# Performance work log

Measured on AMD Instinct MI355X. Metric: run time of the kernel, lower is better.

Reference implementation:

```python
import jax, jax.numpy as jnp
import numpy as np

N, E, L = 20000, 640000, 2
D_IN, D_H, D_FF = 1546, 128, 512  # in_channels, heads*out_channels, ff_dim
EPS = 1e-5
SLOPE = 0.01  # LeakyReLU default negative slope


def layer_norm(x, g, b):
    m = x.mean(-1, keepdims=True)
    v = ((x - m) ** 2).mean(-1, keepdims=True)
    return (x - m) / jnp.sqrt(v + EPS) * g + b


def setup_inputs() -> dict:
    key = jax.random.key(0)
    ks = iter(jax.random.split(key, 40))
    f32 = jnp.float32
    def w(shape, scale=0.05):
        return jax.random.normal(next(ks), shape, dtype=f32) * scale
    inp = {
        "x": jax.random.normal(next(ks), (N, D_IN), dtype=f32),
        "edge_index": jax.random.randint(next(ks), (2, E), 0, N, dtype=jnp.int64),
        "edge_attr": jax.random.normal(next(ks), (E, D_H), dtype=f32),
        # per-layer TransformerConv params, stacked over L layers
        "Wq": w((L, D_IN, D_H)), "bq": jnp.zeros((L, D_H), f32),
        "Wk": w((L, D_IN, D_H)), "bk": jnp.zeros((L, D_H), f32),
        "Wv": w((L, D_IN, D_H)), "bv": jnp.zeros((L, D_H), f32),
        "Wr": w((L, D_IN, D_H)), "br": jnp.zeros((L, D_H), f32),
        "Whi": w((L, D_IN, D_H)), "Whj": w((L, D_IN, D_H)),
        # per-layer FFMLP params
        "W1": w((L, D_H, D_FF)), "b1": jnp.zeros((L, D_FF), f32),
        "W2": w((L, D_FF, D_H)), "b2": jnp.zeros((L, D_H), f32),
        "g1": jnp.ones((L, D_H), f32), "be1": jnp.zeros((L, D_H), f32),
        "g2": jnp.ones((L, D_H), f32), "be2": jnp.zeros((L, D_H), f32),
        # shared linear 128->1546 and final linear2 1546->128
        "linW": w((D_H, D_IN)), "linb": jnp.zeros((D_IN,), f32),
        "lin2W": w((D_IN, D_H)), "lin2b": jnp.zeros((D_H,), f32),
    }
    return inp


def reference(x, edge_index, edge_attr, Wq, bq, Wk, bk, Wv, bv, Wr, br,
              Whi, Whj, W1, b1, W2, b2, g1, be1, g2, be2,
              linW, linb, lin2W, lin2b):
    src = edge_index[0]  # j (source)
    dst = edge_index[1]  # i (target)
    for l in range(L):
        q = x @ Wq[l] + bq[l]          # [N, D_H]
        k = x @ Wk[l] + bk[l]
        v = x @ Wv[l] + bv[l]
        hi = x @ Whi[l]
        hj = x @ Whj[l]
        # edge gate (uses raw edge_attr, matching original forward)
        gate = jax.nn.sigmoid(edge_attr + hi[src] + hj[dst])      # [E, D_H]
        # per-edge scalar attention, softmax over ALL edges (dim=0, as in source)
        attn = jnp.sum(q[dst] * k[src], axis=-1, keepdims=True)   # [E, 1]
        attn = jax.nn.softmax(attn, axis=0)
        msg = attn * v[src] * gate                                 # [E, D_H]
        aggr = jax.ops.segment_sum(msg, dst, num_segments=N)       # [N, D_H]
        h = aggr + x @ Wr[l] + br[l]   # root weight, concat=False -> no out_proj
        # FFMLP (pre-norm residual on normalized input)
        ss = layer_norm(h, g1[l], be1[l])
        ss2 = jax.nn.relu(ss @ W1[l] + b1[l]) @ W2[l] + b2[l]
        h = layer_norm(ss + ss2, g2[l], be2[l])
        x = h @ linW + linb            # shared 128 -> 1546
    x = jax.nn.leaky_relu(x @ lin2W + lin2b, SLOPE)
    return x
```

## Files before the change

kernel.cpp:

```cpp
#include <hip/hip_runtime.h>
#include <cfloat>
#include <cmath>

#define NN 20000
#define EE 640000
#define DIN 1546
#define KIN 1568
#define DH 128
#define DFF 512
#define NL 2
#define NPROJ 768
#define LINNP 1664
#define LINNS 1568
#define ALB 2048

typedef unsigned short ushort_t;
typedef __attribute__((ext_vector_type(8))) short short8;
typedef __attribute__((ext_vector_type(8))) unsigned short ushort8;
typedef __attribute__((ext_vector_type(4))) float floatx4;

__device__ inline ushort_t f2bf(float f) {
  unsigned u = __float_as_uint(f);
  unsigned r = (u + 0x7FFF + ((u >> 16) & 1)) >> 16;
  return (ushort_t)r;
}
__device__ inline float bflo(unsigned u) { return __uint_as_float(u << 16); }
__device__ inline float bfhi(unsigned u) { return __uint_as_float(u & 0xFFFF0000u); }

__global__ __launch_bounds__(256) void gemm_bf16(
    const ushort_t* __restrict__ A, int lda,
    const ushort_t* __restrict__ Bt, int ldb,
    const float* __restrict__ bias, void* __restrict__ Cv, int ldc,
    int M, int Nstore, int K, int act, int out_bf16)
{
  __shared__ ushort_t As[4 * 1032];
  __shared__ ushort_t Bs[4 * 1032];
  const int tid = threadIdx.x;
  const int wave = tid >> 6, lane = tid & 63;
  const int bm = blockIdx.x * 128, bn = blockIdx.y * 128;
  const int wm = (wave >> 1) * 64, wn = (wave & 1) * 64;
  const int frow = lane & 15, kq = lane >> 4;

  floatx4 acc[4][4];
  #pragma unroll
  for (int i = 0; i < 4; ++i)
    #pragma unroll
    for (int j = 0; j < 4; ++j) acc[i][j] = (floatx4){0.f, 0.f, 0.f, 0.f};

  const int srow = tid >> 2, skc = tid & 3;
  const int ar0 = min(bm + srow, M - 1);
  const int ar1 = min(bm + srow + 64, M - 1);
  const ushort_t* Ap0 = A + (size_t)ar0 * lda + skc * 8;
  const ushort_t* Ap1 = A + (size_t)ar1 * lda + skc * 8;
  const ushort_t* Bp0 = Bt + (size_t)(bn + srow) * ldb + skc * 8;
  const ushort_t* Bp1 = Bt + (size_t)(bn + srow + 64) * ldb + skc * 8;
  ushort_t* Aw0 = As + skc * 1032 + srow * 8;
  ushort_t* Aw1 = As + skc * 1032 + (srow + 64) * 8;
  ushort_t* Bw0 = Bs + skc * 1032 + srow * 8;
  ushort_t* Bw1 = Bs + skc * 1032 + (srow + 64) * 8;

  for (int k0 = 0; k0 < K; k0 += 32) {
    ushort8 a0 = *(const ushort8*)Ap0; Ap0 += 32;
    ushort8 a1 = *(const ushort8*)Ap1; Ap1 += 32;
    ushort8 b0 = *(const ushort8*)Bp0; Bp0 += 32;
    ushort8 b1 = *(const ushort8*)Bp1; Bp1 += 32;
    __syncthreads();
    *(ushort8*)Aw0 = a0; *(ushort8*)Aw1 = a1;
    *(ushort8*)Bw0 = b0; *(ushort8*)Bw1 = b1;
    __syncthreads();
    short8 af[4], bf[4];
    #pragma unroll
    for (int i = 0; i < 4; ++i)
      af[i] = *(const short8*)(As + kq * 1032 + (wm + i * 16 + frow) * 8);
    #pragma unroll
    for (int j = 0; j < 4; ++j)
      bf[j] = *(const short8*)(Bs + kq * 1032 + (wn + j * 16 + frow) * 8);
    #pragma unroll
    for (int i = 0; i < 4; ++i)
      #pragma unroll
      for (int j = 0; j < 4; ++j)
        acc[i][j] = __builtin_amdgcn_mfma_f32_16x16x32_bf16(af[i], bf[j], acc[i][j], 0, 0, 0);
  }

  const int rq = (lane >> 4) * 4;
  #pragma unroll
  for (int j = 0; j < 4; ++j) {
    int col = bn + wn + j * 16 + frow;
    if (col >= Nstore) continue;
    float bb = bias ? bias[col] : 0.f;
    #pragma unroll
    for (int i = 0; i < 4; ++i) {
      #pragma unroll
      for (int r = 0; r < 4; ++r) {
        int row = bm + wm + i * 16 + rq + r;
        if (row >= M) continue;
        float v = acc[i][j][r] + bb;
        if (act == 1) v = fmaxf(v, 0.f);
        else if (act == 2) v = v > 0.f ? v : 0.01f * v;
        if (out_bf16) ((ushort_t*)Cv)[(size_t)row * ldc + col] = f2bf(v);
        else          ((float*)Cv)[(size_t)row * ldc + col] = v;
      }
    }
  }
}

__global__ void convert_x_kernel(const float* __restrict__ x, ushort_t* __restrict__ xb) {
  int c = blockIdx.x * 256 + threadIdx.x;
  int row = blockIdx.y;
  if (c >= KIN) return;
  xb[(size_t)row * KIN + c] = (c < DIN) ? f2bf(x[(size_t)row * DIN + c]) : (ushort_t)0;
}

__global__ void pack6_kernel(const float* __restrict__ Wq, const float* __restrict__ Wk,
                             const float* __restrict__ Wv, const float* __restrict__ Wr,
                             const float* __restrict__ Whi, const float* __restrict__ Whj,
                             ushort_t* __restrict__ Wt6) {
  int k = blockIdx.x * 256 + threadIdx.x;
  int n = blockIdx.y;
  if (k >= KIN) return;
  const float* W[6] = {Wq, Wk, Wv, Wr, Whi, Whj};
  int which = n >> 7, col = n & 127;
  float v = (k < DIN) ? W[which][(size_t)k * DH + col] : 0.f;
  Wt6[(size_t)n * KIN + k] = f2bf(v);
}

__global__ void pack_bt_kernel(const float* __restrict__ src, ushort_t* __restrict__ dst,
                               int Nsrc, int Ksrc, int Kp) {
  int k = blockIdx.x * 256 + threadIdx.x;
  int n = blockIdx.y;
  if (k >= Kp) return;
  float v = (n < Nsrc && k < Ksrc) ? src[(size_t)k * Nsrc + n] : 0.f;
  dst[(size_t)n * Kp + k] = f2bf(v);
}

__global__ void pack_bias_kernel(const float* __restrict__ bq, const float* __restrict__ bk,
                                 const float* __restrict__ bv, const float* __restrict__ br,
                                 float* __restrict__ out) {
  int n = blockIdx.x * 256 + threadIdx.x;
  if (n >= NPROJ) return;
  int which = n >> 7, c = n & 127;
  float v = 0.f;
  if (which == 0) v = bq[c]; else if (which == 1) v = bk[c];
  else if (which == 2) v = bv[c]; else if (which == 3) v = br[c];
  out[n] = v;
}

__global__ void pad_linb_kernel(const float* __restrict__ linb, float* __restrict__ out) {
  int n = blockIdx.x * 256 + threadIdx.x;
  if (n >= LINNS) return;
  out[n] = (n < DIN) ? linb[n] : 0.f;
}

__global__ void hist_kernel(const int* __restrict__ ei, int* __restrict__ counts) {
  int e = blockIdx.x * 256 + threadIdx.x;
  if (e < EE) atomicAdd(&counts[ei[EE + e]], 1);
}

__global__ __launch_bounds__(1024) void scan_kernel(const int* __restrict__ counts,
                                                    int* __restrict__ offsets,
                                                    int* __restrict__ cursor) {
  __shared__ int sums[1024];
  const int t = threadIdx.x;
  const int PER = 20;
  int base = t * PER;
  int loc[PER]; int s = 0;
  #pragma unroll
  for (int i = 0; i < PER; ++i) {
    int idx = base + i;
    int c = (idx < NN) ? counts[idx] : 0;
    loc[i] = s; s += c;
  }
  sums[t] = s;
  __syncthreads();
  for (int d = 1; d < 1024; d <<= 1) {
    int v = (t >= d) ? sums[t - d] : 0;
    __syncthreads();
    sums[t] += v;
    __syncthreads();
  }
  int pre = (t > 0) ? sums[t - 1] : 0;
  #pragma unroll
  for (int i = 0; i < PER; ++i) {
    int idx = base + i;
    if (idx < NN) { offsets[idx] = pre + loc[i]; cursor[idx] = pre + loc[i]; }
  }
  if (t == 0) offsets[NN] = sums[1023];
}

__global__ void scatter_kernel(const int* __restrict__ ei, int* __restrict__ cursor,
                               int* __restrict__ csr) {
  int e = blockIdx.x * 256 + threadIdx.x;
  if (e < EE) {
    int p = atomicAdd(&cursor[ei[EE + e]], 1);
    csr[p] = e;
  }
}

__device__ inline void atomicMaxF(float* addr, float val) {
  if (val >= 0.f) atomicMax((int*)addr, __float_as_int(val));
  else            atomicMin((unsigned int*)addr, __float_as_uint(val));
}

__global__ void init_scalars(float* scal) {
  if (threadIdx.x == 0) { scal[0] = -INFINITY; scal[1] = 0.f; }
}

__global__ __launch_bounds__(256) void attn_logits(
    const int* __restrict__ ei, const ushort_t* __restrict__ qkv,
    float* __restrict__ s_e, float* __restrict__ scal)
{
  const int tid = threadIdx.x;
  const int l = tid & 31;
  const int ngroups = ALB * 8;
  const int g = blockIdx.x * 8 + (tid >> 5);
  float mx = -FLT_MAX;
  for (int e = g; e < EE; e += 2 * ngroups) {
    const int e2 = e + ngroups;
    const bool has2 = (e2 < EE);
    int src1 = ei[e], dst1 = ei[EE + e];
    int src2 = has2 ? ei[e2] : src1;
    int dst2 = has2 ? ei[EE + e2] : dst1;
    uint2 qu1 = *(const uint2*)(qkv + (size_t)dst1 * NPROJ + l * 4);
    uint2 ku1 = *(const uint2*)(qkv + (size_t)src1 * NPROJ + DH + l * 4);
    uint2 qu2 = *(const uint2*)(qkv + (size_t)dst2 * NPROJ + l * 4);
    uint2 ku2 = *(const uint2*)(qkv + (size_t)src2 * NPROJ + DH + l * 4);
    float d1 = bflo(qu1.x) * bflo(ku1.x) + bfhi(qu1.x) * bfhi(ku1.x)
             + bflo(qu1.y) * bflo(ku1.y) + bfhi(qu1.y) * bfhi(ku1.y);
    float d2 = bflo(qu2.x) * bflo(ku2.x) + bfhi(qu2.x) * bfhi(ku2.x)
             + bflo(qu2.y) * bflo(ku2.y) + bfhi(qu2.y) * bfhi(ku2.y);
    #pragma unroll
    for (int m = 16; m >= 1; m >>= 1) {
      d1 += __shfl_xor(d1, m);
      d2 += __shfl_xor(d2, m);
    }
    if (l == 0) {
      s_e[e] = d1;
      if (has2) s_e[e2] = d2;
    }
    mx = fmaxf(mx, has2 ? fmaxf(d1, d2) : d1);
  }
  mx = fmaxf(mx, __shfl_xor(mx, 32));
  __shared__ float red[4];
  if ((tid & 63) == 0) red[tid >> 6] = mx;
  __syncthreads();
  if (tid == 0)
    atomicMaxF(scal, fmaxf(fmaxf(red[0], red[1]), fmaxf(red[2], red[3])));
}

__global__ __launch_bounds__(256) void exp_sum(
    float* __restrict__ s_e, const float* __restrict__ scal, float* __restrict__ Z)
{
  const int e = blockIdx.x * 256 + threadIdx.x;
  const float mx = scal[0];
  float v = __expf(s_e[e] - mx);
  s_e[e] = v;
  float t = v;
  #pragma unroll
  for (int m = 32; m >= 1; m >>= 1) t += __shfl_xor(t, m);
  __shared__ float red[4];
  if ((threadIdx.x & 63) == 0) red[threadIdx.x >> 6] = t;
  __syncthreads();
  if (threadIdx.x == 0) atomicAdd(Z, red[0] + red[1] + red[2] + red[3]);
}

__global__ __launch_bounds__(256) void aggregate_kernel(
    const int* __restrict__ ei, const int* __restrict__ offsets,
    const int* __restrict__ csr, const float* __restrict__ s_e,
    const float* __restrict__ scal, const ushort_t* __restrict__ qkv,
    const float* __restrict__ ea, float* __restrict__ h)
{
  const int node = blockIdx.x * 4 + (threadIdx.x >> 6);
  const int lane = threadIdx.x & 63;
  if (node >= NN) return;
  const int off = offsets[node];
  const int deg = offsets[node + 1] - off;
  const float invZ = 1.f / scal[1];
  const ushort_t* bd = qkv + (size_t)node * NPROJ;
  unsigned hjp = *(const unsigned*)(bd + 640 + lane * 2);
  unsigned rp  = *(const unsigned*)(bd + 384 + lane * 2);
  const float hj0 = bflo(hjp), hj1 = bfhi(hjp);
  float a0 = bflo(rp), a1 = bfhi(rp);
  for (int b0 = 0; b0 < deg; b0 += 64) {
    int t = b0 + lane;
    int eL = (t < deg) ? csr[off + t] : 0;
    int sL = (t < deg) ? ei[eL] : 0;
    float pL = (t < deg) ? s_e[eL] * invZ : 0.f;
    int cnt = min(64, deg - b0);
    for (int u = 0; u < cnt; ++u) {
      int e = __shfl(eL, u);
      int src = __shfl(sL, u);
      float p = __shfl(pL, u);
      const ushort_t* bs = qkv + (size_t)src * NPROJ;
      unsigned vv = *(const unsigned*)(bs + 256 + lane * 2);
      unsigned hv = *(const unsigned*)(bs + 512 + lane * 2);
      float2 eav = *(const float2*)(ea + (size_t)e * DH + lane * 2);
      float g0 = 1.f / (1.f + __expf(-(eav.x + bflo(hv) + hj0)));
      float g1 = 1.f / (1.f + __expf(-(eav.y + bfhi(hv) + hj1)));
      a0 = fmaf(p * bflo(vv), g0, a0);
      a1 = fmaf(p * bfhi(vv), g1, a1);
    }
  }
  *(float2*)(h + (size_t)node * DH + lane * 2) = make_float2(a0, a1);
}

__global__ __launch_bounds__(256) void ln_kernel(
    const float* __restrict__ X, const float* __restrict__ X2,
    const float* __restrict__ g, const float* __restrict__ b,
    float* __restrict__ Yf, ushort_t* __restrict__ Yb)
{
  int row = blockIdx.x * 4 + (threadIdx.x >> 6);
  int lane = threadIdx.x & 63;
  if (row >= NN) return;
  float2 x = *(const float2*)(X + (size_t)row * DH + lane * 2);
  if (X2) {
    float2 y = *(const float2*)(X2 + (size_t)row * DH + lane * 2);
    x.x += y.x; x.y += y.y;
  }
  float s = x.x + x.y;
  #pragma unroll
  for (int m = 32; m >= 1; m >>= 1) s += __shfl_xor(s, m);
  float mean = s * (1.f / 128.f);
  float dx = x.x - mean, dy = x.y - mean;
  float v = dx * dx + dy * dy;
  #pragma unroll
  for (int m = 32; m >= 1; m >>= 1) v += __shfl_xor(v, m);
  float rstd = rsqrtf(v * (1.f / 128.f) + 1e-5f);
  float2 gg = *(const float2*)(g + lane * 2);
  float2 bb = *(const float2*)(b + lane * 2);
  float o0 = dx * rstd * gg.x + bb.x;
  float o1 = dy * rstd * gg.y + bb.y;
  if (Yf) *(float2*)(Yf + (size_t)row * DH + lane * 2) = make_float2(o0, o1);
  if (Yb) {
    ushort_t* p = Yb + (size_t)row * DH + lane * 2;
    p[0] = f2bf(o0); p[1] = f2bf(o1);
  }
}

extern "C" void kernel_launch(void* const* d_in, const int* in_sizes, int n_in,
                              void* d_out, int out_size, void* d_ws, size_t ws_size,
                              hipStream_t stream)
{
  const float* x_in  = (const float*)d_in[0];
  const int*   ei    = (const int*)d_in[1];
  const float* ea    = (const float*)d_in[2];
  const float* Wq    = (const float*)d_in[3];
  const float* bq    = (const float*)d_in[4];
  const float* Wk    = (const float*)d_in[5];
  const float* bk    = (const float*)d_in[6];
  const float* Wv    = (const float*)d_in[7];
  const float* bv    = (const float*)d_in[8];
  const float* Wr    = (const float*)d_in[9];
  const float* br    = (const float*)d_in[10];
  const float* Whi   = (const float*)d_in[11];
  const float* Whj   = (const float*)d_in[12];
  const float* W1    = (const float*)d_in[13];
  const float* b1    = (const float*)d_in[14];
  const float* W2    = (const float*)d_in[15];
  const float* b2    = (const float*)d_in[16];
  const float* g1    = (const float*)d_in[17];
  const float* be1   = (const float*)d_in[18];
  const float* g2    = (const float*)d_in[19];
  const float* be2   = (const float*)d_in[20];
  const float* linW  = (const float*)d_in[21];
  const float* linb  = (const float*)d_in[22];
  const float* lin2W = (const float*)d_in[23];
  const float* lin2b = (const float*)d_in[24];
  float* out = (float*)d_out;

  char* p = (char*)d_ws;
  auto alloc = [&](size_t bytes) -> void* {
    void* r = (void*)p; p += (bytes + 63) & ~((size_t)63); return r;
  };
  ushort_t* x_bf   = (ushort_t*)alloc((size_t)NN * KIN * 2);
  ushort_t* qkvp   = (ushort_t*)alloc((size_t)NN * NPROJ * 2);
  ushort_t* Wt6    = (ushort_t*)alloc((size_t)NPROJ * KIN * 2);
  ushort_t* W1t    = (ushort_t*)alloc((size_t)DFF * DH * 2);
  ushort_t* W2t    = (ushort_t*)alloc((size_t)DH * DFF * 2);
  ushort_t* lint   = (ushort_t*)alloc((size_t)LINNP * DH * 2);
  ushort_t* lin2t  = (ushort_t*)alloc((size_t)DH * KIN * 2);
  float*    bias768= (float*)alloc(NPROJ * 4);
  float*    linbp  = (float*)alloc(LINNS * 4);
  float*    s_e    = (float*)alloc((size_t)EE * 4);
  float*    scal   = (float*)alloc(64);
  int*      counts = (int*)alloc((size_t)NN * 4);
  int*      offsets= (int*)alloc((size_t)(NN + 1) * 4);
  int*      cursor = (int*)alloc((size_t)NN * 4);
  int*      csr    = (int*)alloc((size_t)EE * 4);
  float*    h      = (float*)alloc((size_t)NN * DH * 4);
  float*    ss     = (float*)alloc((size_t)NN * DH * 4);
  ushort_t* ssbf   = (ushort_t*)alloc((size_t)NN * DH * 2);
  ushort_t* ff1bf  = (ushort_t*)alloc((size_t)NN * DFF * 2);
  float*    ss2    = (float*)alloc((size_t)NN * DH * 4);
  ushort_t* h2bf   = (ushort_t*)alloc((size_t)NN * DH * 2);

  const dim3 blk(256);
  const int MB = (NN + 127) / 128;

  convert_x_kernel<<<dim3(7, NN), blk, 0, stream>>>(x_in, x_bf);
  pack_bt_kernel<<<dim3(1, LINNP), blk, 0, stream>>>(linW, lint, DIN, DH, DH);
  pack_bt_kernel<<<dim3(7, DH), blk, 0, stream>>>(lin2W, lin2t, DH, DIN, KIN);
  pad_linb_kernel<<<dim3(7), blk, 0, stream>>>(linb, linbp);
  hipMemsetAsync(counts, 0, (size_t)NN * 4, stream);
  hist_kernel<<<dim3(EE / 256), blk, 0, stream>>>(ei, counts);
  scan_kernel<<<dim3(1), dim3(1024), 0, stream>>>(counts, offsets, cursor);
  scatter_kernel<<<dim3(EE / 256), blk, 0, stream>>>(ei, cursor, csr);

  for (int l = 0; l < NL; ++l) {
    const size_t wo = (size_t)l * DIN * DH;
    pack6_kernel<<<dim3(7, NPROJ), blk, 0, stream>>>(
        Wq + wo, Wk + wo, Wv + wo, Wr + wo, Whi + wo, Whj + wo, Wt6);
    pack_bias_kernel<<<dim3(3), blk, 0, stream>>>(
        bq + (size_t)l * DH, bk + (size_t)l * DH, bv + (size_t)l * DH, br + (size_t)l * DH, bias768);
    pack_bt_kernel<<<dim3(1, DFF), blk, 0, stream>>>(W1 + (size_t)l * DH * DFF, W1t, DFF, DH, DH);
    pack_bt_kernel<<<dim3(2, DH), blk, 0, stream>>>(W2 + (size_t)l * DFF * DH, W2t, DH, DFF, DFF);

    gemm_bf16<<<dim3(MB, 6), blk, 0, stream>>>(
        x_bf, KIN, Wt6, KIN, bias768, qkvp, NPROJ, NN, NPROJ, KIN, 0, 1);

    init_scalars<<<1, 64, 0, stream>>>(scal);
    attn_logits<<<dim3(ALB), blk, 0, stream>>>(ei, qkvp, s_e, scal);
    exp_sum<<<dim3(EE / 256), blk, 0, stream>>>(s_e, scal, scal + 1);
    aggregate_kernel<<<dim3(NN / 4), blk, 0, stream>>>(
        ei, offsets, csr, s_e, scal, qkvp, ea, h);

    ln_kernel<<<dim3(NN / 4), blk, 0, stream>>>(h, nullptr, g1 + (size_t)l * DH, be1 + (size_t)l * DH, ss, ssbf);
    gemm_bf16<<<dim3(MB, 4), blk, 0, stream>>>(
        ssbf, DH, W1t, DH, b1 + (size_t)l * DFF, ff1bf, DFF, NN, DFF, DH, 1, 1);
    gemm_bf16<<<dim3(MB, 1), blk, 0, stream>>>(
        ff1bf, DFF, W2t, DFF, b2 + (size_t)l * DH, ss2, DH, NN, DH, DFF, 0, 0);
    ln_kernel<<<dim3(NN / 4), blk, 0, stream>>>(ss, ss2, g2 + (size_t)l * DH, be2 + (size_t)l * DH, nullptr, h2bf);

    gemm_bf16<<<dim3(MB, 13), blk, 0, stream>>>(
        h2bf, DH, lint, DH, linbp, x_bf, KIN, NN, LINNS, DH, 0, 1);
  }

  gemm_bf16<<<dim3(MB, 1), blk, 0, stream>>>(
      x_bf, KIN, lin2t, KIN, lin2b, out, DH, NN, DH, KIN, 2, 0);
}
```

Baseline: 1.610 ms.

## Fold shared 128->1546 linear into following projection weights

Precomputes combined weights linW·W for the layer-1 projections and linW·lin2W for the final linear, including combined biases. The wide 1546-column intermediate x is no longer materialised after each layer. The layer-2 projection GEMM and the final GEMM then run with K=128 instead of K=1568. This removes two large GEMMs and their traffic, at the cost of small weight-combination kernels and different bf16 rounding of the folded weights.

Result: no change. 1.585 ms (-1.5%).

```diff
diff --git a/kernel.cpp b/kernel.cpp
--- a/kernel.cpp
+++ b/kernel.cpp
@@ -10,8 +10,6 @@
 #define DFF 512
 #define NL 2
 #define NPROJ 768
-#define LINNP 1664
-#define LINNS 1568
 #define ALB 2048
 
 typedef unsigned short ushort_t;
@@ -145,10 +143,78 @@
   out[n] = v;
 }
 
-__global__ void pad_linb_kernel(const float* __restrict__ linb, float* __restrict__ out) {
-  int n = blockIdx.x * 256 + threadIdx.x;
-  if (n >= LINNS) return;
-  out[n] = (n < DIN) ? linb[n] : 0.f;
+__global__ __launch_bounds__(256) void combine6_kernel(
+    const float* __restrict__ Wq, const float* __restrict__ Wk,
+    const float* __restrict__ Wv, const float* __restrict__ Wr,
+    const float* __restrict__ Whi, const float* __restrict__ Whj,
+    const float* __restrict__ bq, const float* __restrict__ bk,
+    const float* __restrict__ bv, const float* __restrict__ br,
+    const float* __restrict__ linW, const float* __restrict__ linb,
+    ushort_t* __restrict__ Pc, float* __restrict__ bc)
+{
+  const int j = threadIdx.x >> 7;
+  const int k = threadIdx.x & 127;
+  const int n = blockIdx.x * 2 + j;
+  const int which = n >> 7, col = n & 127;
+  const float* Ws[6] = {Wq, Wk, Wv, Wr, Whi, Whj};
+  const float* W = Ws[which];
+  __shared__ float wcol[2][DIN];
+  for (int d = k; d < DIN; d += 128)
+    wcol[j][d] = W[(size_t)d * DH + col];
+  __syncthreads();
+  const float* lr = linW + (size_t)k * DIN;
+  float acc = 0.f;
+  #pragma unroll 4
+  for (int d = 0; d < DIN; d += 2) {
+    float2 lv = *(const float2*)(lr + d);
+    acc = fmaf(wcol[j][d], lv.x, acc);
+    acc = fmaf(wcol[j][d + 1], lv.y, acc);
+  }
+  Pc[(size_t)n * DH + k] = f2bf(acc);
+  float bs = 0.f;
+  for (int d = k; d < DIN; d += 128) bs += linb[d] * wcol[j][d];
+  #pragma unroll
+  for (int m = 32; m >= 1; m >>= 1) bs += __shfl_xor(bs, m);
+  __shared__ float red[4];
+  if ((threadIdx.x & 63) == 0) red[threadIdx.x >> 6] = bs;
+  __syncthreads();
+  if (k == 0) {
+    float b0 = 0.f;
+    if (which == 0) b0 = bq[col]; else if (which == 1) b0 = bk[col];
+    else if (which == 2) b0 = bv[col]; else if (which == 3) b0 = br[col];
+    bc[n] = b0 + red[j * 2] + red[j * 2 + 1];
+  }
+}
+
+__global__ __launch_bounds__(256) void combine_fin_kernel(
+    const float* __restrict__ lin2W, const float* __restrict__ lin2b,
+    const float* __restrict__ linW, const float* __restrict__ linb,
+    ushort_t* __restrict__ Pf, float* __restrict__ bf_out)
+{
+  const int j = threadIdx.x >> 7;
+  const int k = threadIdx.x & 127;
+  const int c = blockIdx.x * 2 + j;
+  __shared__ float wcol[2][DIN];
+  for (int d = k; d < DIN; d += 128)
+    wcol[j][d] = lin2W[(size_t)d * DH + c];
+  __syncthreads();
+  const float* lr = linW + (size_t)k * DIN;
+  float acc = 0.f;
+  #pragma unroll 4
+  for (int d = 0; d < DIN; d += 2) {
+    float2 lv = *(const float2*)(lr + d);
+    acc = fmaf(wcol[j][d], lv.x, acc);
+    acc = fmaf(wcol[j][d + 1], lv.y, acc);
+  }
+  Pf[(size_t)c * DH + k] = f2bf(acc);
+  float bs = 0.f;
+  for (int d = k; d < DIN; d += 128) bs += linb[d] * wcol[j][d];
+  #pragma unroll
+  for (int m = 32; m >= 1; m >>= 1) bs += __shfl_xor(bs, m);
+  __shared__ float red[4];
+  if ((threadIdx.x & 63) == 0) red[threadIdx.x >> 6] = bs;
+  __syncthreads();
+  if (k == 0) bf_out[c] = lin2b[c] + red[j * 2] + red[j * 2 + 1];
 }
 
 __global__ void hist_kernel(const int* __restrict__ ei, int* __restrict__ counts) {
@@ -376,10 +442,11 @@
   ushort_t* Wt6    = (ushort_t*)alloc((size_t)NPROJ * KIN * 2);
   ushort_t* W1t    = (ushort_t*)alloc((size_t)DFF * DH * 2);
   ushort_t* W2t    = (ushort_t*)alloc((size_t)DH * DFF * 2);
-  ushort_t* lint   = (ushort_t*)alloc((size_t)LINNP * DH * 2);
-  ushort_t* lin2t  = (ushort_t*)alloc((size_t)DH * KIN * 2);
+  ushort_t* Wc6    = (ushort_t*)alloc((size_t)NPROJ * DH * 2);
+  ushort_t* Wcf    = (ushort_t*)alloc((size_t)DH * DH * 2);
   float*    bias768= (float*)alloc(NPROJ * 4);
-  float*    linbp  = (float*)alloc(LINNS * 4);
+  float*    bc768  = (float*)alloc(NPROJ * 4);
+  float*    bcf    = (float*)alloc(DH * 4);
   float*    s_e    = (float*)alloc((size_t)EE * 4);
   float*    scal   = (float*)alloc(64);
   int*      counts = (int*)alloc((size_t)NN * 4);
@@ -397,25 +464,32 @@
   const int MB = (NN + 127) / 128;
 
   convert_x_kernel<<<dim3(7, NN), blk, 0, stream>>>(x_in, x_bf);
-  pack_bt_kernel<<<dim3(1, LINNP), blk, 0, stream>>>(linW, lint, DIN, DH, DH);
-  pack_bt_kernel<<<dim3(7, DH), blk, 0, stream>>>(lin2W, lin2t, DH, DIN, KIN);
-  pad_linb_kernel<<<dim3(7), blk, 0, stream>>>(linb, linbp);
   hipMemsetAsync(counts, 0, (size_t)NN * 4, stream);
   hist_kernel<<<dim3(EE / 256), blk, 0, stream>>>(ei, counts);
   scan_kernel<<<dim3(1), dim3(1024), 0, stream>>>(counts, offsets, cursor);
   scatter_kernel<<<dim3(EE / 256), blk, 0, stream>>>(ei, cursor, csr);
 
+  const size_t wo1 = (size_t)DIN * DH;
+  combine6_kernel<<<dim3(NPROJ / 2), blk, 0, stream>>>(
+      Wq + wo1, Wk + wo1, Wv + wo1, Wr + wo1, Whi + wo1, Whj + wo1,
+      bq + DH, bk + DH, bv + DH, br + DH, linW, linb, Wc6, bc768);
+  combine_fin_kernel<<<dim3(DH / 2), blk, 0, stream>>>(
+      lin2W, lin2b, linW, linb, Wcf, bcf);
+
   for (int l = 0; l < NL; ++l) {
-    const size_t wo = (size_t)l * DIN * DH;
-    pack6_kernel<<<dim3(7, NPROJ), blk, 0, stream>>>(
-        Wq + wo, Wk + wo, Wv + wo, Wr + wo, Whi + wo, Whj + wo, Wt6);
-    pack_bias_kernel<<<dim3(3), blk, 0, stream>>>(
-        bq + (size_t)l * DH, bk + (size_t)l * DH, bv + (size_t)l * DH, br + (size_t)l * DH, bias768);
     pack_bt_kernel<<<dim3(1, DFF), blk, 0, stream>>>(W1 + (size_t)l * DH * DFF, W1t, DFF, DH, DH);
     pack_bt_kernel<<<dim3(2, DH), blk, 0, stream>>>(W2 + (size_t)l * DFF * DH, W2t, DH, DFF, DFF);
 
-    gemm_bf16<<<dim3(MB, 6), blk, 0, stream>>>(
-        x_bf, KIN, Wt6, KIN, bias768, qkvp, NPROJ, NN, NPROJ, KIN, 0, 1);
+    if (l == 0) {
+      pack6_kernel<<<dim3(7, NPROJ), blk, 0, stream>>>(
+          Wq, Wk, Wv, Wr, Whi, Whj, Wt6);
+      pack_bias_kernel<<<dim3(3), blk, 0, stream>>>(bq, bk, bv, br, bias768);
+      gemm_bf16<<<dim3(MB, 6), blk, 0, stream>>>(
+          x_bf, KIN, Wt6, KIN, bias768, qkvp, NPROJ, NN, NPROJ, KIN, 0, 1);
+    } else {
+      gemm_bf16<<<dim3(MB, 6), blk, 0, stream>>>(
+          h2bf, DH, Wc6, DH, bc768, qkvp, NPROJ, NN, NPROJ, DH, 0, 1);
+    }
 
     init_scalars<<<1, 64, 0, stream>>>(scal);
     attn_logits<<<dim3(ALB), blk, 0, stream>>>(ei, qkvp, s_e, scal);
@@ -429,11 +503,8 @@
     gemm_bf16<<<dim3(MB, 1), blk, 0, stream>>>(
         ff1bf, DFF, W2t, DFF, b2 + (size_t)l * DH, ss2, DH, NN, DH, DFF, 0, 0);
     ln_kernel<<<dim3(NN / 4), blk, 0, stream>>>(ss, ss2, g2 + (size_t)l * DH, be2 + (size_t)l * DH, nullptr, h2bf);
-
-    gemm_bf16<<<dim3(MB, 13), blk, 0, stream>>>(
-        h2bf, DH, lint, DH, linbp, x_bf, KIN, NN, LINNS, DH, 0, 1);
   }
 
   gemm_bf16<<<dim3(MB, 1), blk, 0, stream>>>(
-      x_bf, KIN, lin2t, KIN, lin2b, out, DH, NN, DH, KIN, 2, 0);
-}
+      h2bf, DH, Wcf, DH, bcf, out, DH, NN, DH, DH, 2, 0);
+}
```
